# Kernel optimization log

Hardware: AMD Instinct MI355X
Metric: run time of the kernel (lower is better)

Reference implementation:

```python
import jax, jax.numpy as jnp
import numpy as np

B, S, H = 32, 2048, 1024


def setup_inputs() -> dict:
    key = jax.random.key(0)
    k1, k2, k3, k4, k5, k6 = jax.random.split(key, 6)
    sc = 1.0 / np.sqrt(H)
    return {
        "dec_state": jax.random.normal(k1, (B, 1, H), dtype=jnp.float32),
        "enc_state": jax.random.normal(k2, (B, S, 2 * H), dtype=jnp.float32),
        "src_length": jax.random.randint(k3, (B,), 1, S + 1, dtype=jnp.int32),
        "W_enc": jax.random.normal(k4, (H, 2 * H), dtype=jnp.float32) * sc,
        "W_dec": jax.random.normal(k5, (H, H), dtype=jnp.float32) * sc,
        "W_energy": jax.random.normal(k6, (1, H), dtype=jnp.float32) * sc,
    }


def reference(dec_state, enc_state, src_length, W_enc, W_dec, W_energy):
    # enc: [B,S,H], dec: [B,1,H]
    enc = jnp.einsum('bse,he->bsh', enc_state, W_enc)
    dec = jnp.einsum('bod,hd->boh', dec_state, W_dec)
    # energies: [B,S] -> [B,1,S]
    energies = jnp.einsum('bsh,oh->bso', jnp.tanh(dec + enc), W_energy)[..., 0]
    mask = jnp.arange(S)[None, :] < src_length[:, None]  # [B,S]
    energies = jnp.where(mask, energies, -jnp.inf)[:, None, :]  # [B,1,S]
    alphas = jax.nn.softmax(energies, axis=-1)
    context = jnp.einsum('bos,se->boe', alphas[:, 0:1, :].squeeze(1)[:, None, :].squeeze(1)[:, None, :].squeeze(1)[:, None, :], enc_state) if False else jnp.matmul(alphas, enc_state)  # [B,1,2H]
    return context, alphas
```

## Files before the change

kernel.cpp:

```cpp
#include <hip/hip_runtime.h>
#include <hip/hip_bf16.h>
#include <stdint.h>

#define B_  32
#define S_  2048
#define H_  1024
#define K_  2048
#define M_  65536

#define BM  128
#define BN  128
#define BK  32
#define LDK 40

typedef __bf16 bf16x8 __attribute__((ext_vector_type(8)));
typedef float  f32x4  __attribute__((ext_vector_type(4)));

__device__ __forceinline__ unsigned short f2bf(float x) {
    unsigned u = __builtin_bit_cast(unsigned, x);
    u += 0x7fffu + ((u >> 16) & 1u);
    return (unsigned short)(u >> 16);
}

__device__ __forceinline__ unsigned pk_bf16(float x, float y) {
#if __has_builtin(__builtin_amdgcn_cvt_pk_bf16_f32)
    auto r = __builtin_amdgcn_cvt_pk_bf16_f32(x, y);
    static_assert(sizeof(r) == 4, "cvt_pk_bf16 size");
    return __builtin_bit_cast(unsigned, r);
#else
    return ((unsigned)f2bf(x)) | ((unsigned)f2bf(y) << 16);
#endif
}

__device__ __forceinline__ float bf2f(unsigned u16) {
    return __builtin_bit_cast(float, u16 << 16);
}

__device__ __forceinline__ float tanh_fast(float x) {
    float e = __expf(2.0f * x);
    return 1.0f - 2.0f / (e + 1.0f);
}

__global__ __launch_bounds__(256) void cast8_k(const float* __restrict__ in,
                                               unsigned short* __restrict__ o, long n8) {
    long i = (long)blockIdx.x * 256 + threadIdx.x;
    if (i < n8) {
        const float4* p = (const float4*)(in + i * 8);
        float4 a = p[0], b = p[1];
        uint4 pk;
        pk.x = pk_bf16(a.x, a.y);
        pk.y = pk_bf16(a.z, a.w);
        pk.z = pk_bf16(b.x, b.y);
        pk.w = pk_bf16(b.z, b.w);
        *(uint4*)(o + i * 8) = pk;
    }
}

__global__ __launch_bounds__(256) void dec_k(const float* __restrict__ ds,
                                             const float* __restrict__ Wd,
                                             float* __restrict__ decv) {
    const int b = blockIdx.y;
    const int w = threadIdx.x >> 6, lane = threadIdx.x & 63;
    const int h = blockIdx.x * 4 + w;
    const float* wr = Wd + (long)h * H_;
    const float* dr = ds + (long)b * H_;
    float acc = 0.f;
#pragma unroll
    for (int i = 0; i < 4; i++) {
        int idx = lane * 4 + i * 256;
        float4 a = *(const float4*)(wr + idx);
        float4 d = *(const float4*)(dr + idx);
        acc += a.x * d.x + a.y * d.y + a.z * d.z + a.w * d.w;
    }
    for (int m2 = 1; m2 < 64; m2 <<= 1) acc += __shfl_xor(acc, m2, 64);
    if (lane == 0) decv[(long)b * H_ + h] = acc;
}

__device__ __forceinline__ void energy_epilogue(f32x4 acc[4][4], int mb, int nb,
                                                const float* decv, const float* Weng,
                                                float* pe, float esum[2][BM],
                                                int t, int wm, int wn, int r, int g) {
    const int b = mb >> 4;
    float wv[4], dv[4];
#pragma unroll
    for (int ni = 0; ni < 4; ni++) {
        int h = nb * BN + wn * 64 + ni * 16 + r;
        wv[ni] = Weng[h];
        dv[ni] = decv[b * H_ + h];
    }
    float rs[4][4];
#pragma unroll
    for (int mi = 0; mi < 4; mi++)
#pragma unroll
        for (int rr = 0; rr < 4; rr++) rs[mi][rr] = 0.f;
#pragma unroll
    for (int mi = 0; mi < 4; mi++)
#pragma unroll
        for (int ni = 0; ni < 4; ni++)
#pragma unroll
            for (int rr = 0; rr < 4; rr++)
                rs[mi][rr] += wv[ni] * tanh_fast(dv[ni] + acc[mi][ni][rr]);
#pragma unroll
    for (int m2 = 1; m2 < 16; m2 <<= 1)
#pragma unroll
        for (int mi = 0; mi < 4; mi++)
#pragma unroll
            for (int rr = 0; rr < 4; rr++)
                rs[mi][rr] += __shfl_xor(rs[mi][rr], m2, 64);
    if (r == 0) {
#pragma unroll
        for (int mi = 0; mi < 4; mi++)
#pragma unroll
            for (int rr = 0; rr < 4; rr++)
                esum[wn][wm * 64 + mi * 16 + g * 4 + rr] = rs[mi][rr];
    }
    __syncthreads();
    if (t < BM) pe[(long)nb * M_ + (long)mb * BM + t] = esum[0][t] + esum[1][t];
}

__global__ __launch_bounds__(256) void gemm_fast(const unsigned short* __restrict__ Abf,
                                                 const unsigned short* __restrict__ Bw,
                                                 const float* __restrict__ decv,
                                                 const float* __restrict__ Weng,
                                                 float* __restrict__ pe) {
    __shared__ __align__(1024) unsigned short Asm[BM * BK];
    __shared__ __align__(1024) unsigned short Bsm[BN * BK];
    __shared__ float esum[2][BM];

    const int L = blockIdx.x;
    const int xcd = L & 7;
    const int slot = L >> 3;
    const int nb = slot & 7;
    const int mb = (slot >> 3) * 8 + xcd;

    const int t = threadIdx.x;
    const int lane = t & 63, w = t >> 6;
    const int wm = w >> 1, wn = w & 1;
    const int r = lane & 15, g = lane >> 4;

    f32x4 acc[4][4];
#pragma unroll
    for (int mi = 0; mi < 4; mi++)
#pragma unroll
        for (int ni = 0; ni < 4; ni++)
#pragma unroll
            for (int k = 0; k < 4; k++) acc[mi][ni][k] = 0.f;

    const unsigned short* Abase = Abf + (long)mb * BM * K_;
    const unsigned short* Bbase = Bw + (long)nb * BN * K_;

    for (int kt = 0; kt < K_; kt += BK) {
        __syncthreads();
#pragma unroll
        for (int j = 0; j < 2; j++) {
            int u = t + 256 * j;
            int row = u >> 2, c8 = (u & 3) << 3;
            __builtin_amdgcn_global_load_lds(
                (const __attribute__((address_space(1))) unsigned*)(Abase + (long)row * K_ + kt + c8),
                (__attribute__((address_space(3))) unsigned*)&Asm[u * 8], 16, 0, 0);
        }
#pragma unroll
        for (int j = 0; j < 2; j++) {
            int u = t + 256 * j;
            int row = u >> 2, c8 = (u & 3) << 3;
            __builtin_amdgcn_global_load_lds(
                (const __attribute__((address_space(1))) unsigned*)(Bbase + (long)row * K_ + kt + c8),
                (__attribute__((address_space(3))) unsigned*)&Bsm[u * 8], 16, 0, 0);
        }
        __syncthreads();
        bf16x8 af[4], bfr[4];
#pragma unroll
        for (int mi = 0; mi < 4; mi++)
            af[mi] = *(const bf16x8*)&Asm[(wm * 64 + mi * 16 + r) * BK + g * 8];
#pragma unroll
        for (int ni = 0; ni < 4; ni++)
            bfr[ni] = *(const bf16x8*)&Bsm[(wn * 64 + ni * 16 + r) * BK + g * 8];
#pragma unroll
        for (int mi = 0; mi < 4; mi++)
#pragma unroll
            for (int ni = 0; ni < 4; ni++)
                acc[mi][ni] = __builtin_amdgcn_mfma_f32_16x16x32_bf16(af[mi], bfr[ni],
                                                                     acc[mi][ni], 0, 0, 0);
    }
    energy_epilogue(acc, mb, nb, decv, Weng, pe, esum, t, wm, wn, r, g);
}

__global__ __launch_bounds__(256) void gemm_energy(const float* __restrict__ A,
                                                   const unsigned short* __restrict__ Bw,
                                                   const float* __restrict__ decv,
                                                   const float* __restrict__ Weng,
                                                   float* __restrict__ pe) {
    __shared__ __align__(16) unsigned short Asm[BM * LDK];
    __shared__ __align__(1024) unsigned short Bsm[BN * BK];
    __shared__ float esum[2][BM];

    const int L = blockIdx.x;
    const int xcd = L & 7;
    const int slot = L >> 3;
    const int nb = slot & 7;
    const int mb = (slot >> 3) * 8 + xcd;

    const int t = threadIdx.x;
    const int lane = t & 63, w = t >> 6;
    const int wm = w >> 1, wn = w & 1;
    const int r = lane & 15, g = lane >> 4;

    f32x4 acc[4][4];
#pragma unroll
    for (int mi = 0; mi < 4; mi++)
#pragma unroll
        for (int ni = 0; ni < 4; ni++)
#pragma unroll
            for (int k = 0; k < 4; k++) acc[mi][ni][k] = 0.f;

    const float* Abase = A + (long)mb * BM * K_;
    const unsigned short* Bbase = Bw + (long)nb * BN * K_;

    for (int kt = 0; kt < K_; kt += BK) {
        __syncthreads();
#pragma unroll
        for (int j = 0; j < 2; j++) {
            int u = t + 256 * j;
            int row = u >> 2, c8 = (u & 3) << 3;
            __builtin_amdgcn_global_load_lds(
                (const __attribute__((address_space(1))) unsigned*)(Bbase + (long)row * K_ + kt + c8),
                (__attribute__((address_space(3))) unsigned*)&Bsm[u * 8], 16, 0, 0);
        }
#pragma unroll
        for (int i = 0; i < 4; i++) {
            int f = t + 256 * i;
            int row = f >> 3, c4 = (f & 7) << 2;
            float4 v = *(const float4*)(Abase + (long)row * K_ + kt + c4);
            uint2 pk;
            pk.x = pk_bf16(v.x, v.y);
            pk.y = pk_bf16(v.z, v.w);
            *(uint2*)&Asm[row * LDK + c4] = pk;
        }
        __syncthreads();
        bf16x8 af[4], bfr[4];
#pragma unroll
        for (int mi = 0; mi < 4; mi++)
            af[mi] = *(const bf16x8*)&Asm[(wm * 64 + mi * 16 + r) * LDK + g * 8];
#pragma unroll
        for (int ni = 0; ni < 4; ni++)
            bfr[ni] = *(const bf16x8*)&Bsm[(wn * 64 + ni * 16 + r) * BK + g * 8];
#pragma unroll
        for (int mi = 0; mi < 4; mi++)
#pragma unroll
            for (int ni = 0; ni < 4; ni++)
                acc[mi][ni] = __builtin_amdgcn_mfma_f32_16x16x32_bf16(af[mi], bfr[ni],
                                                                     acc[mi][ni], 0, 0, 0);
    }
    energy_epilogue(acc, mb, nb, decv, Weng, pe, esum, t, wm, wn, r, g);
}

__global__ __launch_bounds__(256) void softmax_k(const float* __restrict__ pe,
                                                 const int* __restrict__ slen,
                                                 float* __restrict__ alph) {
    const int b = blockIdx.x, t = threadIdx.x;
    const int len = slen[b];
    __shared__ float sh[4];
    const float NEG = -__builtin_inff();
    float e[8];
    float mx = NEG;
#pragma unroll
    for (int i = 0; i < 8; i++) {
        int s = t + i * 256;
        float v = 0.f;
#pragma unroll
        for (int p = 0; p < 8; p++) v += pe[(long)p * M_ + b * S_ + s];
        v = (s < len) ? v : NEG;
        e[i] = v;
        mx = fmaxf(mx, v);
    }
    for (int m2 = 1; m2 < 64; m2 <<= 1) mx = fmaxf(mx, __shfl_xor(mx, m2, 64));
    if ((t & 63) == 0) sh[t >> 6] = mx;
    __syncthreads();
    mx = fmaxf(fmaxf(sh[0], sh[1]), fmaxf(sh[2], sh[3]));
    float sum = 0.f;
#pragma unroll
    for (int i = 0; i < 8; i++) {
        float x = (e[i] == NEG) ? 0.f : __expf(e[i] - mx);
        e[i] = x;
        sum += x;
    }
    for (int m2 = 1; m2 < 64; m2 <<= 1) sum += __shfl_xor(sum, m2, 64);
    __syncthreads();
    if ((t & 63) == 0) sh[t >> 6] = sum;
    __syncthreads();
    sum = sh[0] + sh[1] + sh[2] + sh[3];
    float inv = 1.0f / sum;
#pragma unroll
    for (int i = 0; i < 8; i++) alph[b * S_ + t + i * 256] = e[i] * inv;
}

__global__ __launch_bounds__(256) void context_bf(const unsigned short* __restrict__ encbf,
                                                  const float* __restrict__ alph,
                                                  const int* __restrict__ slen,
                                                  float* __restrict__ out) {
    const int slot = blockIdx.x;
    const int b = slot & 31, sc = slot >> 5;
    const int len = slen[b];
    const int s0 = sc * 64;
    if (s0 >= len) return;
    const int send = min(s0 + 64, len);
    __shared__ float al[64];
    const int t = threadIdx.x;
    if (t < 64) al[t] = alph[b * S_ + s0 + t];
    __syncthreads();
    const unsigned short* base = encbf + ((long)b * S_ + s0) * K_ + t * 8;
    float ac[8];
#pragma unroll
    for (int j = 0; j < 8; j++) ac[j] = 0.f;
#pragma unroll 4
    for (int s = s0; s < send; ++s) {
        float a = al[s - s0];
        uint4 v = *(const uint4*)base;
        ac[0] += a * bf2f(v.x & 0xffffu);
        ac[1] += a * bf2f(v.x >> 16);
        ac[2] += a * bf2f(v.y & 0xffffu);
        ac[3] += a * bf2f(v.y >> 16);
        ac[4] += a * bf2f(v.z & 0xffffu);
        ac[5] += a * bf2f(v.z >> 16);
        ac[6] += a * bf2f(v.w & 0xffffu);
        ac[7] += a * bf2f(v.w >> 16);
        base += K_;
    }
    float* o = out + (long)b * K_ + t * 8;
#pragma unroll
    for (int j = 0; j < 8; j++) atomicAdd(o + j, ac[j]);
}

__global__ __launch_bounds__(256) void context_f32(const float* __restrict__ enc,
                                                   const float* __restrict__ alph,
                                                   const int* __restrict__ slen,
                                                   float* __restrict__ out) {
    const int slot = blockIdx.x;
    const int b = slot & 31, ec = (slot >> 5) & 1, sc = slot >> 6;
    const int len = slen[b];
    const int s0 = sc * 64;
    if (s0 >= len) return;
    const int send = min(s0 + 64, len);
    __shared__ float al[64];
    const int t = threadIdx.x;
    if (t < 64) al[t] = alph[b * S_ + s0 + t];
    __syncthreads();
    const int e0 = ec * 1024 + t * 4;
    const float* base = enc + ((long)b * S_ + s0) * K_ + e0;
    float ax = 0.f, ay = 0.f, az = 0.f, aw = 0.f;
#pragma unroll 4
    for (int s = s0; s < send; ++s) {
        float a = al[s - s0];
        float4 v = *(const float4*)base;
        ax += a * v.x; ay += a * v.y; az += a * v.z; aw += a * v.w;
        base += K_;
    }
    float* o = out + (long)b * K_ + e0;
    atomicAdd(o + 0, ax);
    atomicAdd(o + 1, ay);
    atomicAdd(o + 2, az);
    atomicAdd(o + 3, aw);
}

extern "C" void kernel_launch(void* const* d_in, const int* in_sizes, int n_in,
                              void* d_out, int out_size, void* d_ws, size_t ws_size,
                              hipStream_t stream) {
    const float* dec_state = (const float*)d_in[0];
    const float* enc_state = (const float*)d_in[1];
    const int*   src_len   = (const int*)d_in[2];
    const float* W_enc     = (const float*)d_in[3];
    const float* W_dec     = (const float*)d_in[4];
    const float* W_energy  = (const float*)d_in[5];
    float* out = (float*)d_out;

    char* ws = (char*)d_ws;
    float* decv = (float*)ws;
    float* pe   = (float*)(ws + (1 << 17));
    unsigned short* Wenc_bf = (unsigned short*)(ws + 3 * (1 << 20));
    unsigned short* Abf = (unsigned short*)(ws + 8 * (1 << 20));
    float* alph = out + 65536;

    const size_t need_fast = 8ull * (1 << 20) + (size_t)M_ * K_ * 2;

    hipMemsetAsync(out, 0, 65536 * sizeof(float), stream);

    cast8_k<<<1024, 256, 0, stream>>>(W_enc, Wenc_bf, (long)H_ * K_ / 8);
    dec_k<<<dim3(H_ / 4, B_), 256, 0, stream>>>(dec_state, W_dec, decv);

    if (ws_size >= need_fast) {
        cast8_k<<<65536, 256, 0, stream>>>(enc_state, Abf, (long)M_ * K_ / 8);
        gemm_fast<<<4096, 256, 0, stream>>>(Abf, Wenc_bf, decv, W_energy, pe);
        softmax_k<<<B_, 256, 0, stream>>>(pe, src_len, alph);
        context_bf<<<1024, 256, 0, stream>>>(Abf, alph, src_len, out);
    } else {
        gemm_energy<<<4096, 256, 0, stream>>>(enc_state, Wenc_bf, decv, W_energy, pe);
        softmax_k<<<B_, 256, 0, stream>>>(pe, src_len, alph);
        context_f32<<<2048, 256, 0, stream>>>(enc_state, alph, src_len, out);
    }
}
```

Before: 1.131 ms.

## Rewrite bf16 energy GEMM with 256x256 tiles and 4-stage LDS pipeline

Replaces the 128x128 single-buffered GEMM with a 512-thread, 256x256-tile kernel. It uses a 4-slot LDS ring of direct global-to-LDS loads with explicit vmcnt waits, split barriers and MFMA priority raising, so loads overlap compute and operand reuse per block doubles. With only 4 N-blocks, the softmax now sums 4 partial energy planes instead of 8, halving that traffic. The cast kernel becomes grid-stride with fewer blocks. The risks are higher register pressure from 32 accumulators and a tighter hand-scheduled pipeline with less occupancy.

Result: no change. 1.117 ms (-1.3%).

```diff
diff --git a/kernel.cpp b/kernel.cpp
--- a/kernel.cpp
+++ b/kernel.cpp
@@ -43,8 +43,8 @@
 
 __global__ __launch_bounds__(256) void cast8_k(const float* __restrict__ in,
                                                unsigned short* __restrict__ o, long n8) {
-    long i = (long)blockIdx.x * 256 + threadIdx.x;
-    if (i < n8) {
+    const long stride = (long)gridDim.x * 256;
+    for (long i = (long)blockIdx.x * 256 + threadIdx.x; i < n8; i += stride) {
         const float4* p = (const float4*)(in + i * 8);
         float4 a = p[0], b = p[1];
         uint4 pk;
@@ -118,71 +118,169 @@
     if (t < BM) pe[(long)nb * M_ + (long)mb * BM + t] = esum[0][t] + esum[1][t];
 }
 
-__global__ __launch_bounds__(256) void gemm_fast(const unsigned short* __restrict__ Abf,
-                                                 const unsigned short* __restrict__ Bw,
-                                                 const float* __restrict__ decv,
-                                                 const float* __restrict__ Weng,
-                                                 float* __restrict__ pe) {
-    __shared__ __align__(1024) unsigned short Asm[BM * BK];
-    __shared__ __align__(1024) unsigned short Bsm[BN * BK];
-    __shared__ float esum[2][BM];
+#define GBM 256
+#define GBN 256
+
+#define LDA_(SLOT, RB) (*(const bf16x8*)&LDS[(SLOT) * 8192 + ((RB) * 64 + lane) * 8])
+#define LDB_(SLOT, RB) (*(const bf16x8*)&LDS[32768 + (SLOT) * 8192 + ((RB) * 64 + lane) * 8])
+
+#define STAGE_A(KOFF, SLOT) do { \
+    __builtin_amdgcn_global_load_lds((const __attribute__((address_space(1))) unsigned*)(aQ + (KOFF)), \
+        (__attribute__((address_space(3))) unsigned*)&LDS[(SLOT) * 8192 + t * 8], 16, 0, 0); \
+    __builtin_amdgcn_global_load_lds((const __attribute__((address_space(1))) unsigned*)(aQ2 + (KOFF)), \
+        (__attribute__((address_space(3))) unsigned*)&LDS[(SLOT) * 8192 + 4096 + t * 8], 16, 0, 0); \
+} while (0)
+
+#define STAGE_B(KOFF, SLOT) do { \
+    __builtin_amdgcn_global_load_lds((const __attribute__((address_space(1))) unsigned*)(bQ + (KOFF)), \
+        (__attribute__((address_space(3))) unsigned*)&LDS[32768 + (SLOT) * 8192 + t * 8], 16, 0, 0); \
+    __builtin_amdgcn_global_load_lds((const __attribute__((address_space(1))) unsigned*)(bQ2 + (KOFF)), \
+        (__attribute__((address_space(3))) unsigned*)&LDS[32768 + (SLOT) * 8192 + 4096 + t * 8], 16, 0, 0); \
+} while (0)
+
+#define NOSTAGE do {} while (0)
+#define WAIT4 asm volatile("s_waitcnt vmcnt(4)" ::: "memory")
+#define WAIT0 asm volatile("s_waitcnt vmcnt(0)" ::: "memory")
+#define NOWAIT do {} while (0)
+
+#define PHASE(SLOT, MH, LOADB, STG, WSTMT) do { \
+    bf16x8 a0 = LDA_(SLOT, WR8 + (MH) * 4 + 0); \
+    bf16x8 a1 = LDA_(SLOT, WR8 + (MH) * 4 + 1); \
+    bf16x8 a2 = LDA_(SLOT, WR8 + (MH) * 4 + 2); \
+    bf16x8 a3 = LDA_(SLOT, WR8 + (MH) * 4 + 3); \
+    if (LOADB) { \
+        bq0 = LDB_(SLOT, WC4 + 0); \
+        bq1 = LDB_(SLOT, WC4 + 1); \
+        bq2 = LDB_(SLOT, WC4 + 2); \
+        bq3 = LDB_(SLOT, WC4 + 3); \
+    } \
+    STG; \
+    __builtin_amdgcn_s_barrier(); \
+    __builtin_amdgcn_s_setprio(1); \
+    acc[(MH)*4+0][0] = __builtin_amdgcn_mfma_f32_16x16x32_bf16(a0, bq0, acc[(MH)*4+0][0], 0, 0, 0); \
+    acc[(MH)*4+0][1] = __builtin_amdgcn_mfma_f32_16x16x32_bf16(a0, bq1, acc[(MH)*4+0][1], 0, 0, 0); \
+    acc[(MH)*4+0][2] = __builtin_amdgcn_mfma_f32_16x16x32_bf16(a0, bq2, acc[(MH)*4+0][2], 0, 0, 0); \
+    acc[(MH)*4+0][3] = __builtin_amdgcn_mfma_f32_16x16x32_bf16(a0, bq3, acc[(MH)*4+0][3], 0, 0, 0); \
+    acc[(MH)*4+1][0] = __builtin_amdgcn_mfma_f32_16x16x32_bf16(a1, bq0, acc[(MH)*4+1][0], 0, 0, 0); \
+    acc[(MH)*4+1][1] = __builtin_amdgcn_mfma_f32_16x16x32_bf16(a1, bq1, acc[(MH)*4+1][1], 0, 0, 0); \
+    acc[(MH)*4+1][2] = __builtin_amdgcn_mfma_f32_16x16x32_bf16(a1, bq2, acc[(MH)*4+1][2], 0, 0, 0); \
+    acc[(MH)*4+1][3] = __builtin_amdgcn_mfma_f32_16x16x32_bf16(a1, bq3, acc[(MH)*4+1][3], 0, 0, 0); \
+    acc[(MH)*4+2][0] = __builtin_amdgcn_mfma_f32_16x16x32_bf16(a2, bq0, acc[(MH)*4+2][0], 0, 0, 0); \
+    acc[(MH)*4+2][1] = __builtin_amdgcn_mfma_f32_16x16x32_bf16(a2, bq1, acc[(MH)*4+2][1], 0, 0, 0); \
+    acc[(MH)*4+2][2] = __builtin_amdgcn_mfma_f32_16x16x32_bf16(a2, bq2, acc[(MH)*4+2][2], 0, 0, 0); \
+    acc[(MH)*4+2][3] = __builtin_amdgcn_mfma_f32_16x16x32_bf16(a2, bq3, acc[(MH)*4+2][3], 0, 0, 0); \
+    acc[(MH)*4+3][0] = __builtin_amdgcn_mfma_f32_16x16x32_bf16(a3, bq0, acc[(MH)*4+3][0], 0, 0, 0); \
+    acc[(MH)*4+3][1] = __builtin_amdgcn_mfma_f32_16x16x32_bf16(a3, bq1, acc[(MH)*4+3][1], 0, 0, 0); \
+    acc[(MH)*4+3][2] = __builtin_amdgcn_mfma_f32_16x16x32_bf16(a3, bq2, acc[(MH)*4+3][2], 0, 0, 0); \
+    acc[(MH)*4+3][3] = __builtin_amdgcn_mfma_f32_16x16x32_bf16(a3, bq3, acc[(MH)*4+3][3], 0, 0, 0); \
+    __builtin_amdgcn_s_setprio(0); \
+    WSTMT; \
+    __builtin_amdgcn_s_barrier(); \
+} while (0)
+
+__global__ __launch_bounds__(512, 2) void gemm_fast(const unsigned short* __restrict__ Abf,
+                                                    const unsigned short* __restrict__ Bw,
+                                                    const float* __restrict__ decv,
+                                                    const float* __restrict__ Weng,
+                                                    float* __restrict__ pe) {
+    __shared__ __align__(1024) unsigned short LDS[65536];
 
     const int L = blockIdx.x;
     const int xcd = L & 7;
-    const int slot = L >> 3;
-    const int nb = slot & 7;
-    const int mb = (slot >> 3) * 8 + xcd;
+    const int sl = L >> 3;
+    const int nb = sl & 3;
+    const int mb = (sl >> 2) * 8 + xcd;
 
     const int t = threadIdx.x;
-    const int lane = t & 63, w = t >> 6;
-    const int wm = w >> 1, wn = w & 1;
-    const int r = lane & 15, g = lane >> 4;
-
-    f32x4 acc[4][4];
-#pragma unroll
-    for (int mi = 0; mi < 4; mi++)
+    const int lane = t & 63;
+    const int w = t >> 6;
+    const int WR = w >> 2, WC = w & 3;
+    const int WR8 = WR * 8, WC4 = WC * 4;
+    const int r = lane & 15, g = (lane >> 4) & 3;
+
+    f32x4 acc[8][4];
+#pragma unroll
+    for (int mi = 0; mi < 8; mi++)
 #pragma unroll
         for (int ni = 0; ni < 4; ni++)
 #pragma unroll
             for (int k = 0; k < 4; k++) acc[mi][ni][k] = 0.f;
-
-    const unsigned short* Abase = Abf + (long)mb * BM * K_;
-    const unsigned short* Bbase = Bw + (long)nb * BN * K_;
-
-    for (int kt = 0; kt < K_; kt += BK) {
-        __syncthreads();
-#pragma unroll
-        for (int j = 0; j < 2; j++) {
-            int u = t + 256 * j;
-            int row = u >> 2, c8 = (u & 3) << 3;
-            __builtin_amdgcn_global_load_lds(
-                (const __attribute__((address_space(1))) unsigned*)(Abase + (long)row * K_ + kt + c8),
-                (__attribute__((address_space(3))) unsigned*)&Asm[u * 8], 16, 0, 0);
-        }
-#pragma unroll
-        for (int j = 0; j < 2; j++) {
-            int u = t + 256 * j;
-            int row = u >> 2, c8 = (u & 3) << 3;
-            __builtin_amdgcn_global_load_lds(
-                (const __attribute__((address_space(1))) unsigned*)(Bbase + (long)row * K_ + kt + c8),
-                (__attribute__((address_space(3))) unsigned*)&Bsm[u * 8], 16, 0, 0);
-        }
-        __syncthreads();
-        bf16x8 af[4], bfr[4];
-#pragma unroll
-        for (int mi = 0; mi < 4; mi++)
-            af[mi] = *(const bf16x8*)&Asm[(wm * 64 + mi * 16 + r) * BK + g * 8];
+    bf16x8 bq0, bq1, bq2, bq3;
+
+    const int srow = ((t >> 6) << 4) + (t & 15);
+    const int scol = ((t >> 4) & 3) << 3;
+    const unsigned short* aQ  = Abf + (long)(mb * GBM + srow) * K_ + scol;
+    const unsigned short* aQ2 = aQ + 128L * K_;
+    const unsigned short* bQ  = Bw + (long)(nb * GBN + srow) * K_ + scol;
+    const unsigned short* bQ2 = bQ + 128L * K_;
+
+    STAGE_A(0, 0);   STAGE_B(0, 0);
+    STAGE_A(32, 1);  STAGE_B(32, 1);
+    STAGE_A(64, 2);  STAGE_B(64, 2);
+    WAIT4;
+    __builtin_amdgcn_s_barrier();
+
+#pragma unroll 1
+    for (int i = 0; i < 15; ++i) {
+        PHASE(0, 0, 1, STAGE_A(96, 3), NOWAIT);
+        PHASE(0, 1, 0, STAGE_B(96, 3), WAIT4);
+        PHASE(1, 0, 1, STAGE_A(128, 0), NOWAIT);
+        PHASE(1, 1, 0, STAGE_B(128, 0), WAIT4);
+        PHASE(2, 0, 1, STAGE_A(160, 1), NOWAIT);
+        PHASE(2, 1, 0, STAGE_B(160, 1), WAIT4);
+        PHASE(3, 0, 1, STAGE_A(192, 2), NOWAIT);
+        PHASE(3, 1, 0, STAGE_B(192, 2), WAIT4);
+        aQ += 128; aQ2 += 128; bQ += 128; bQ2 += 128;
+    }
+    PHASE(0, 0, 1, STAGE_A(96, 3), NOWAIT);
+    PHASE(0, 1, 0, STAGE_B(96, 3), WAIT4);
+    PHASE(1, 0, 1, NOSTAGE, NOWAIT);
+    PHASE(1, 1, 0, NOSTAGE, WAIT0);
+    PHASE(2, 0, 1, NOSTAGE, NOWAIT);
+    PHASE(2, 1, 0, NOSTAGE, NOWAIT);
+    PHASE(3, 0, 1, NOSTAGE, NOWAIT);
+    PHASE(3, 1, 0, NOSTAGE, NOWAIT);
+
+    const int b = mb >> 3;
+    float wv[4], dv[4];
+#pragma unroll
+    for (int ni = 0; ni < 4; ni++) {
+        int h = nb * GBN + WC4 * 16 + ni * 16 + r;
+        wv[ni] = Weng[h];
+        dv[ni] = decv[b * H_ + h];
+    }
+    float rs[8][4];
+#pragma unroll
+    for (int mi = 0; mi < 8; mi++)
+#pragma unroll
+        for (int rr = 0; rr < 4; rr++) rs[mi][rr] = 0.f;
+#pragma unroll
+    for (int mi = 0; mi < 8; mi++)
 #pragma unroll
         for (int ni = 0; ni < 4; ni++)
-            bfr[ni] = *(const bf16x8*)&Bsm[(wn * 64 + ni * 16 + r) * BK + g * 8];
-#pragma unroll
-        for (int mi = 0; mi < 4; mi++)
-#pragma unroll
-            for (int ni = 0; ni < 4; ni++)
-                acc[mi][ni] = __builtin_amdgcn_mfma_f32_16x16x32_bf16(af[mi], bfr[ni],
-                                                                     acc[mi][ni], 0, 0, 0);
-    }
-    energy_epilogue(acc, mb, nb, decv, Weng, pe, esum, t, wm, wn, r, g);
+#pragma unroll
+            for (int rr = 0; rr < 4; rr++)
+                rs[mi][rr] += wv[ni] * tanh_fast(dv[ni] + acc[mi][ni][rr]);
+#pragma unroll
+    for (int m2 = 1; m2 < 16; m2 <<= 1)
+#pragma unroll
+        for (int mi = 0; mi < 8; mi++)
+#pragma unroll
+            for (int rr = 0; rr < 4; rr++)
+                rs[mi][rr] += __shfl_xor(rs[mi][rr], m2, 64);
+    float* esumF = (float*)&LDS[0];
+    if (r == 0) {
+#pragma unroll
+        for (int mi = 0; mi < 8; mi++)
+#pragma unroll
+            for (int rr = 0; rr < 4; rr++)
+                esumF[WC * 256 + WR * 128 + mi * 16 + g * 4 + rr] = rs[mi][rr];
+    }
+    __syncthreads();
+    if (t < 256) {
+        float s = esumF[t] + esumF[256 + t] + esumF[512 + t] + esumF[768 + t];
+        pe[(long)nb * M_ + (long)mb * 256 + t] = s;
+    }
 }
 
 __global__ __launch_bounds__(256) void gemm_energy(const float* __restrict__ A,
@@ -256,7 +354,7 @@
 
 __global__ __launch_bounds__(256) void softmax_k(const float* __restrict__ pe,
                                                  const int* __restrict__ slen,
-                                                 float* __restrict__ alph) {
+                                                 float* __restrict__ alph, int np) {
     const int b = blockIdx.x, t = threadIdx.x;
     const int len = slen[b];
     __shared__ float sh[4];
@@ -267,8 +365,7 @@
     for (int i = 0; i < 8; i++) {
         int s = t + i * 256;
         float v = 0.f;
-#pragma unroll
-        for (int p = 0; p < 8; p++) v += pe[(long)p * M_ + b * S_ + s];
+        for (int p = 0; p < np; p++) v += pe[(long)p * M_ + b * S_ + s];
         v = (s < len) ? v : NEG;
         e[i] = v;
         mx = fmaxf(mx, v);
@@ -388,13 +485,13 @@
     dec_k<<<dim3(H_ / 4, B_), 256, 0, stream>>>(dec_state, W_dec, decv);
 
     if (ws_size >= need_fast) {
-        cast8_k<<<65536, 256, 0, stream>>>(enc_state, Abf, (long)M_ * K_ / 8);
-        gemm_fast<<<4096, 256, 0, stream>>>(Abf, Wenc_bf, decv, W_energy, pe);
-        softmax_k<<<B_, 256, 0, stream>>>(pe, src_len, alph);
+        cast8_k<<<2048, 256, 0, stream>>>(enc_state, Abf, (long)M_ * K_ / 8);
+        gemm_fast<<<1024, 512, 0, stream>>>(Abf, Wenc_bf, decv, W_energy, pe);
+        softmax_k<<<B_, 256, 0, stream>>>(pe, src_len, alph, 4);
         context_bf<<<1024, 256, 0, stream>>>(Abf, alph, src_len, out);
     } else {
         gemm_energy<<<4096, 256, 0, stream>>>(enc_state, Wenc_bf, decv, W_energy, pe);
-        softmax_k<<<B_, 256, 0, stream>>>(pe, src_len, alph);
+        softmax_k<<<B_, 256, 0, stream>>>(pe, src_len, alph, 8);
         context_f32<<<2048, 256, 0, stream>>>(enc_state, alph, src_len, out);
     }
 }
```

## Fuse fp32-to-bf16 cast into a software-pipelined GEMM and drop bf16 encoder copy

Applied to the files above, without the earlier changes.

Removes the separate pass that cast the whole encoder tensor to bf16, along with the bf16-based context kernel. The GEMM now reads fp32 encoder rows directly, converts them in registers, and writes them into a triple-buffered LDS ring. B fragments are double-buffered in registers and prefetched one step ahead, using a single barrier per step and raised priority around the MFMAs. The context kernel now reads fp32 encoder data, which costs more bandwidth there but avoids writing and re-reading a large bf16 copy.

After: 1.400 ms. 1.24x slower.

```diff
diff --git a/kernel.cpp b/kernel.cpp
--- a/kernel.cpp
+++ b/kernel.cpp
@@ -7,11 +7,6 @@
 #define H_  1024
 #define K_  2048
 #define M_  65536
-
-#define BM  128
-#define BN  128
-#define BK  32
-#define LDK 40
 
 typedef __bf16 bf16x8 __attribute__((ext_vector_type(8)));
 typedef float  f32x4  __attribute__((ext_vector_type(4)));
@@ -32,10 +27,6 @@
 #endif
 }
 
-__device__ __forceinline__ float bf2f(unsigned u16) {
-    return __builtin_bit_cast(float, u16 << 16);
-}
-
 __device__ __forceinline__ float tanh_fast(float x) {
     float e = __expf(2.0f * x);
     return 1.0f - 2.0f / (e + 1.0f);
@@ -43,8 +34,8 @@
 
 __global__ __launch_bounds__(256) void cast8_k(const float* __restrict__ in,
                                                unsigned short* __restrict__ o, long n8) {
-    long i = (long)blockIdx.x * 256 + threadIdx.x;
-    if (i < n8) {
+    const long stride = (long)gridDim.x * 256;
+    for (long i = (long)blockIdx.x * 256 + threadIdx.x; i < n8; i += stride) {
         const float4* p = (const float4*)(in + i * 8);
         float4 a = p[0], b = p[1];
         uint4 pk;
@@ -76,15 +67,124 @@
     if (lane == 0) decv[(long)b * H_ + h] = acc;
 }
 
-__device__ __forceinline__ void energy_epilogue(f32x4 acc[4][4], int mb, int nb,
-                                                const float* decv, const float* Weng,
-                                                float* pe, float esum[2][BM],
-                                                int t, int wm, int wn, int r, int g) {
+__global__ __launch_bounds__(256, 3) void gemm_fast(const float* __restrict__ A,
+                                                    const unsigned short* __restrict__ Bw,
+                                                    const float* __restrict__ decv,
+                                                    const float* __restrict__ Weng,
+                                                    float* __restrict__ pe) {
+    __shared__ __align__(1024) unsigned short LDS[12288];
+
+    const int L = blockIdx.x;
+    const int xcd = L & 7;
+    const int sl = L >> 3;
+    const int nb = sl & 7;
+    const int mb = (sl >> 3) * 8 + xcd;
+
+    const int t = threadIdx.x;
+    const int lane = t & 63;
+    const int w = t >> 6;
+    const int WR = w >> 1, WC = w & 1;
+    const int r = lane & 15, g = (lane >> 4) & 3;
+
+    f32x4 acc[4][4];
+#pragma unroll
+    for (int mi = 0; mi < 4; mi++)
+#pragma unroll
+        for (int ni = 0; ni < 4; ni++)
+#pragma unroll
+            for (int k = 0; k < 4; k++) acc[mi][ni][k] = 0.f;
+
+    const int R = t >> 1, ch = t & 1;
+    const float* aCur = A + (long)(mb * 128 + R) * K_ + ch * 16;
+    const int wrE = (((R >> 4) << 6) + ((ch * 2) << 4) + (R & 15)) * 8;
+    const int rdE = (((WR * 4) << 6) + (g << 4) + r) * 8;
+
+    const unsigned short* bCur = Bw + (long)(nb * 128 + WC * 64 + r) * K_ + g * 8;
+
+    float4 sa0, sa1, sa2, sa3;
+    bf16x8 bqA0, bqA1, bqA2, bqA3, bqB0, bqB1, bqB2, bqB3;
+    int srd = 0;
+
+#define STAGEWR(SLOT) do { \
+    uint4 w0, w1; \
+    w0.x = pk_bf16(sa0.x, sa0.y); w0.y = pk_bf16(sa0.z, sa0.w); \
+    w0.z = pk_bf16(sa1.x, sa1.y); w0.w = pk_bf16(sa1.z, sa1.w); \
+    w1.x = pk_bf16(sa2.x, sa2.y); w1.y = pk_bf16(sa2.z, sa2.w); \
+    w1.z = pk_bf16(sa3.x, sa3.y); w1.w = pk_bf16(sa3.z, sa3.w); \
+    *(uint4*)&LDS[(SLOT) * 4096 + wrE] = w0; \
+    *(uint4*)&LDS[(SLOT) * 4096 + wrE + 128] = w1; \
+} while (0)
+
+#define LOADA do { \
+    sa0 = *(const float4*)(aCur); sa1 = *(const float4*)(aCur + 4); \
+    sa2 = *(const float4*)(aCur + 8); sa3 = *(const float4*)(aCur + 12); \
+    aCur += 32; \
+} while (0)
+
+#define LOADB(Q) do { \
+    Q##0 = *(const bf16x8*)(bCur); \
+    Q##1 = *(const bf16x8*)(bCur + 16 * K_); \
+    Q##2 = *(const bf16x8*)(bCur + 32 * K_); \
+    Q##3 = *(const bf16x8*)(bCur + 48 * K_); \
+    bCur += 32; \
+} while (0)
+
+#define MF(Av, Bv, C) __builtin_amdgcn_mfma_f32_16x16x32_bf16((Av), (Bv), (C), 0, 0, 0)
+
+#define PHASE(BQC, BQN, DO_WR, DO_A, DO_B) do { \
+    int swr = srd + 1; if (swr == 3) swr = 0; \
+    if (DO_WR) STAGEWR(swr); \
+    if (DO_A) LOADA; \
+    if (DO_B) LOADB(BQN); \
+    asm volatile("s_waitcnt lgkmcnt(0)" ::: "memory"); \
+    __builtin_amdgcn_s_barrier(); \
+    { \
+        bf16x8 a0 = *(const bf16x8*)&LDS[srd * 4096 + rdE]; \
+        bf16x8 a1 = *(const bf16x8*)&LDS[srd * 4096 + rdE + 512]; \
+        bf16x8 a2 = *(const bf16x8*)&LDS[srd * 4096 + rdE + 1024]; \
+        bf16x8 a3 = *(const bf16x8*)&LDS[srd * 4096 + rdE + 1536]; \
+        __builtin_amdgcn_s_setprio(1); \
+        acc[0][0] = MF(a0, BQC##0, acc[0][0]); \
+        acc[0][1] = MF(a0, BQC##1, acc[0][1]); \
+        acc[0][2] = MF(a0, BQC##2, acc[0][2]); \
+        acc[0][3] = MF(a0, BQC##3, acc[0][3]); \
+        acc[1][0] = MF(a1, BQC##0, acc[1][0]); \
+        acc[1][1] = MF(a1, BQC##1, acc[1][1]); \
+        acc[1][2] = MF(a1, BQC##2, acc[1][2]); \
+        acc[1][3] = MF(a1, BQC##3, acc[1][3]); \
+        acc[2][0] = MF(a2, BQC##0, acc[2][0]); \
+        acc[2][1] = MF(a2, BQC##1, acc[2][1]); \
+        acc[2][2] = MF(a2, BQC##2, acc[2][2]); \
+        acc[2][3] = MF(a2, BQC##3, acc[2][3]); \
+        acc[3][0] = MF(a3, BQC##0, acc[3][0]); \
+        acc[3][1] = MF(a3, BQC##1, acc[3][1]); \
+        acc[3][2] = MF(a3, BQC##2, acc[3][2]); \
+        acc[3][3] = MF(a3, BQC##3, acc[3][3]); \
+        __builtin_amdgcn_s_setprio(0); \
+    } \
+    srd = swr; \
+} while (0)
+
+    LOADA;
+    STAGEWR(0);
+    LOADA;
+    LOADB(bqA);
+    asm volatile("s_waitcnt lgkmcnt(0)" ::: "memory");
+    __builtin_amdgcn_s_barrier();
+
+#pragma unroll 1
+    for (int i = 0; i < 31; ++i) {
+        PHASE(bqA, bqB, 1, 1, 1);
+        PHASE(bqB, bqA, 1, 1, 1);
+    }
+    PHASE(bqA, bqB, 1, 0, 1);
+    PHASE(bqB, bqA, 0, 0, 0);
+
     const int b = mb >> 4;
     float wv[4], dv[4];
 #pragma unroll
     for (int ni = 0; ni < 4; ni++) {
-        int h = nb * BN + wn * 64 + ni * 16 + r;
+        int h = nb * 128 + WC * 64 + ni * 16 + r;
         wv[ni] = Weng[h];
         dv[ni] = decv[b * H_ + h];
     }
@@ -107,156 +207,24 @@
 #pragma unroll
             for (int rr = 0; rr < 4; rr++)
                 rs[mi][rr] += __shfl_xor(rs[mi][rr], m2, 64);
+    __syncthreads();
+    float* esumF = (float*)&LDS[0];
     if (r == 0) {
 #pragma unroll
         for (int mi = 0; mi < 4; mi++)
 #pragma unroll
             for (int rr = 0; rr < 4; rr++)
-                esum[wn][wm * 64 + mi * 16 + g * 4 + rr] = rs[mi][rr];
-    }
-    __syncthreads();
-    if (t < BM) pe[(long)nb * M_ + (long)mb * BM + t] = esum[0][t] + esum[1][t];
-}
-
-__global__ __launch_bounds__(256) void gemm_fast(const unsigned short* __restrict__ Abf,
-                                                 const unsigned short* __restrict__ Bw,
-                                                 const float* __restrict__ decv,
-                                                 const float* __restrict__ Weng,
-                                                 float* __restrict__ pe) {
-    __shared__ __align__(1024) unsigned short Asm[BM * BK];
-    __shared__ __align__(1024) unsigned short Bsm[BN * BK];
-    __shared__ float esum[2][BM];
-
-    const int L = blockIdx.x;
-    const int xcd = L & 7;
-    const int slot = L >> 3;
-    const int nb = slot & 7;
-    const int mb = (slot >> 3) * 8 + xcd;
-
-    const int t = threadIdx.x;
-    const int lane = t & 63, w = t >> 6;
-    const int wm = w >> 1, wn = w & 1;
-    const int r = lane & 15, g = lane >> 4;
-
-    f32x4 acc[4][4];
-#pragma unroll
-    for (int mi = 0; mi < 4; mi++)
-#pragma unroll
-        for (int ni = 0; ni < 4; ni++)
-#pragma unroll
-            for (int k = 0; k < 4; k++) acc[mi][ni][k] = 0.f;
-
-    const unsigned short* Abase = Abf + (long)mb * BM * K_;
-    const unsigned short* Bbase = Bw + (long)nb * BN * K_;
-
-    for (int kt = 0; kt < K_; kt += BK) {
-        __syncthreads();
-#pragma unroll
-        for (int j = 0; j < 2; j++) {
-            int u = t + 256 * j;
-            int row = u >> 2, c8 = (u & 3) << 3;
-            __builtin_amdgcn_global_load_lds(
-                (const __attribute__((address_space(1))) unsigned*)(Abase + (long)row * K_ + kt + c8),
-                (__attribute__((address_space(3))) unsigned*)&Asm[u * 8], 16, 0, 0);
-        }
-#pragma unroll
-        for (int j = 0; j < 2; j++) {
-            int u = t + 256 * j;
-            int row = u >> 2, c8 = (u & 3) << 3;
-            __builtin_amdgcn_global_load_lds(
-                (const __attribute__((address_space(1))) unsigned*)(Bbase + (long)row * K_ + kt + c8),
-                (__attribute__((address_space(3))) unsigned*)&Bsm[u * 8], 16, 0, 0);
-        }
-        __syncthreads();
-        bf16x8 af[4], bfr[4];
-#pragma unroll
-        for (int mi = 0; mi < 4; mi++)
-            af[mi] = *(const bf16x8*)&Asm[(wm * 64 + mi * 16 + r) * BK + g * 8];
-#pragma unroll
-        for (int ni = 0; ni < 4; ni++)
-            bfr[ni] = *(const bf16x8*)&Bsm[(wn * 64 + ni * 16 + r) * BK + g * 8];
-#pragma unroll
-        for (int mi = 0; mi < 4; mi++)
-#pragma unroll
-            for (int ni = 0; ni < 4; ni++)
-                acc[mi][ni] = __builtin_amdgcn_mfma_f32_16x16x32_bf16(af[mi], bfr[ni],
-                                                                     acc[mi][ni], 0, 0, 0);
-    }
-    energy_epilogue(acc, mb, nb, decv, Weng, pe, esum, t, wm, wn, r, g);
-}
-
-__global__ __launch_bounds__(256) void gemm_energy(const float* __restrict__ A,
-                                                   const unsigned short* __restrict__ Bw,
-                                                   const float* __restrict__ decv,
-                                                   const float* __restrict__ Weng,
-                                                   float* __restrict__ pe) {
-    __shared__ __align__(16) unsigned short Asm[BM * LDK];
-    __shared__ __align__(1024) unsigned short Bsm[BN * BK];
-    __shared__ float esum[2][BM];
-
-    const int L = blockIdx.x;
-    const int xcd = L & 7;
-    const int slot = L >> 3;
-    const int nb = slot & 7;
-    const int mb = (slot >> 3) * 8 + xcd;
-
-    const int t = threadIdx.x;
-    const int lane = t & 63, w = t >> 6;
-    const int wm = w >> 1, wn = w & 1;
-    const int r = lane & 15, g = lane >> 4;
-
-    f32x4 acc[4][4];
-#pragma unroll
-    for (int mi = 0; mi < 4; mi++)
-#pragma unroll
-        for (int ni = 0; ni < 4; ni++)
-#pragma unroll
-            for (int k = 0; k < 4; k++) acc[mi][ni][k] = 0.f;
-
-    const float* Abase = A + (long)mb * BM * K_;
-    const unsigned short* Bbase = Bw + (long)nb * BN * K_;
-
-    for (int kt = 0; kt < K_; kt += BK) {
-        __syncthreads();
-#pragma unroll
-        for (int j = 0; j < 2; j++) {
-            int u = t + 256 * j;
-            int row = u >> 2, c8 = (u & 3) << 3;
-            __builtin_amdgcn_global_load_lds(
-                (const __attribute__((address_space(1))) unsigned*)(Bbase + (long)row * K_ + kt + c8),
-                (__attribute__((address_space(3))) unsigned*)&Bsm[u * 8], 16, 0, 0);
-        }
-#pragma unroll
-        for (int i = 0; i < 4; i++) {
-            int f = t + 256 * i;
-            int row = f >> 3, c4 = (f & 7) << 2;
-            float4 v = *(const float4*)(Abase + (long)row * K_ + kt + c4);
-            uint2 pk;
-            pk.x = pk_bf16(v.x, v.y);
-            pk.y = pk_bf16(v.z, v.w);
-            *(uint2*)&Asm[row * LDK + c4] = pk;
-        }
-        __syncthreads();
-        bf16x8 af[4], bfr[4];
-#pragma unroll
-        for (int mi = 0; mi < 4; mi++)
-            af[mi] = *(const bf16x8*)&Asm[(wm * 64 + mi * 16 + r) * LDK + g * 8];
-#pragma unroll
-        for (int ni = 0; ni < 4; ni++)
-            bfr[ni] = *(const bf16x8*)&Bsm[(wn * 64 + ni * 16 + r) * BK + g * 8];
-#pragma unroll
-        for (int mi = 0; mi < 4; mi++)
-#pragma unroll
-            for (int ni = 0; ni < 4; ni++)
-                acc[mi][ni] = __builtin_amdgcn_mfma_f32_16x16x32_bf16(af[mi], bfr[ni],
-                                                                     acc[mi][ni], 0, 0, 0);
-    }
-    energy_epilogue(acc, mb, nb, decv, Weng, pe, esum, t, wm, wn, r, g);
+                esumF[WC * 128 + WR * 64 + mi * 16 + g * 4 + rr] = rs[mi][rr];
+    }
+    __syncthreads();
+    if (t < 128) {
+        pe[(long)nb * M_ + (long)mb * 128 + t] = esumF[t] + esumF[128 + t];
+    }
 }
 
 __global__ __launch_bounds__(256) void softmax_k(const float* __restrict__ pe,
                                                  const int* __restrict__ slen,
-                                                 float* __restrict__ alph) {
+                                                 float* __restrict__ alph, int np) {
     const int b = blockIdx.x, t = threadIdx.x;
     const int len = slen[b];
     __shared__ float sh[4];
@@ -267,8 +235,7 @@
     for (int i = 0; i < 8; i++) {
         int s = t + i * 256;
         float v = 0.f;
-#pragma unroll
-        for (int p = 0; p < 8; p++) v += pe[(long)p * M_ + b * S_ + s];
+        for (int p = 0; p < np; p++) v += pe[(long)p * M_ + b * S_ + s];
         v = (s < len) ? v : NEG;
         e[i] = v;
         mx = fmaxf(mx, v);
@@ -292,43 +259,6 @@
     float inv = 1.0f / sum;
 #pragma unroll
     for (int i = 0; i < 8; i++) alph[b * S_ + t + i * 256] = e[i] * inv;
-}
-
-__global__ __launch_bounds__(256) void context_bf(const unsigned short* __restrict__ encbf,
-                                                  const float* __restrict__ alph,
-                                                  const int* __restrict__ slen,
-                                                  float* __restrict__ out) {
-    const int slot = blockIdx.x;
-    const int b = slot & 31, sc = slot >> 5;
-    const int len = slen[b];
-    const int s0 = sc * 64;
-    if (s0 >= len) return;
-    const int send = min(s0 + 64, len);
-    __shared__ float al[64];
-    const int t = threadIdx.x;
-    if (t < 64) al[t] = alph[b * S_ + s0 + t];
-    __syncthreads();
-    const unsigned short* base = encbf + ((long)b * S_ + s0) * K_ + t * 8;
-    float ac[8];
-#pragma unroll
-    for (int j = 0; j < 8; j++) ac[j] = 0.f;
-#pragma unroll 4
-    for (int s = s0; s < send; ++s) {
-        float a = al[s - s0];
-        uint4 v = *(const uint4*)base;
-        ac[0] += a * bf2f(v.x & 0xffffu);
-        ac[1] += a * bf2f(v.x >> 16);
-        ac[2] += a * bf2f(v.y & 0xffffu);
-        ac[3] += a * bf2f(v.y >> 16);
-        ac[4] += a * bf2f(v.z & 0xffffu);
-        ac[5] += a * bf2f(v.z >> 16);
-        ac[6] += a * bf2f(v.w & 0xffffu);
-        ac[7] += a * bf2f(v.w >> 16);
-        base += K_;
-    }
-    float* o = out + (long)b * K_ + t * 8;
-#pragma unroll
-    for (int j = 0; j < 8; j++) atomicAdd(o + j, ac[j]);
 }
 
 __global__ __launch_bounds__(256) void context_f32(const float* __restrict__ enc,
@@ -377,24 +307,14 @@
     float* decv = (float*)ws;
     float* pe   = (float*)(ws + (1 << 17));
     unsigned short* Wenc_bf = (unsigned short*)(ws + 3 * (1 << 20));
-    unsigned short* Abf = (unsigned short*)(ws + 8 * (1 << 20));
     float* alph = out + 65536;
-
-    const size_t need_fast = 8ull * (1 << 20) + (size_t)M_ * K_ * 2;
 
     hipMemsetAsync(out, 0, 65536 * sizeof(float), stream);
 
     cast8_k<<<1024, 256, 0, stream>>>(W_enc, Wenc_bf, (long)H_ * K_ / 8);
     dec_k<<<dim3(H_ / 4, B_), 256, 0, stream>>>(dec_state, W_dec, decv);
 
-    if (ws_size >= need_fast) {
-        cast8_k<<<65536, 256, 0, stream>>>(enc_state, Abf, (long)M_ * K_ / 8);
-        gemm_fast<<<4096, 256, 0, stream>>>(Abf, Wenc_bf, decv, W_energy, pe);
-        softmax_k<<<B_, 256, 0, stream>>>(pe, src_len, alph);
-        context_bf<<<1024, 256, 0, stream>>>(Abf, alph, src_len, out);
-    } else {
-        gemm_energy<<<4096, 256, 0, stream>>>(enc_state, Wenc_bf, decv, W_energy, pe);
-        softmax_k<<<B_, 256, 0, stream>>>(pe, src_len, alph);
-        context_f32<<<2048, 256, 0, stream>>>(enc_state, alph, src_len, out);
-    }
-}
+    gemm_fast<<<4096, 256, 0, stream>>>(enc_state, Wenc_bf, decv, W_energy, pe);
+    softmax_k<<<B_, 256, 0, stream>>>(pe, src_len, alph, 8);
+    context_f32<<<2048, 256, 0, stream>>>(enc_state, alph, src_len, out);
+}
```
